# Kernel tuning notes

Measured on AMD Instinct MI355X. Metric: run time of the kernel, lower is better.

Reference implementation:

```python
import jax, jax.numpy as jnp
import numpy as np

B = 262144
L, NO, NW = 5, 5, 3          # num_layers, num_ops, num_widths
AD = L * NO * NW             # arch_dim = 75
D, H = 64, 4                 # embed_dim, num_heads
HD = D // H                  # head_dim = 16
EPS = 1e-5


def _ln(x, g, b):
    m = x.mean(-1, keepdims=True)
    v = ((x - m) ** 2).mean(-1, keepdims=True)
    return (x - m) / jnp.sqrt(v + EPS) * g + b


def setup_inputs() -> dict:
    key = jax.random.key(0)
    ks = jax.random.split(key, 16)
    s = 0.05
    return {
        "hw_idx": jax.random.randint(ks[0], (B,), 0, 4),
        "op_indices": jax.random.randint(ks[1], (B, L), 0, NO),
        "width_indices": jax.random.randint(ks[2], (B, L), 0, NW),
        "hw_embed": jax.random.normal(ks[3], (4, D)) * s,
        "W1": jax.random.normal(ks[4], (128, AD)) * s, "b1": jnp.zeros((128,)),
        "W2": jax.random.normal(ks[5], (D, 128)) * s, "b2": jnp.zeros((D,)),
        "ln1_g": jnp.ones((D,)), "ln1_b": jnp.zeros((D,)),
        "in_proj_w": jax.random.normal(ks[6], (3 * D, D)) * s,
        "in_proj_b": jnp.zeros((3 * D,)),
        "out_proj_w": jax.random.normal(ks[7], (D, D)) * s,
        "out_proj_b": jnp.zeros((D,)),
        "ln2_g": jnp.ones((D,)), "ln2_b": jnp.zeros((D,)),
        "W3": jax.random.normal(ks[8], (32, D)) * s, "b3": jnp.zeros((32,)),
        "W4": jax.random.normal(ks[9], (1, 32)) * s, "b4": jnp.zeros((1,)),
    }


def reference(hw_idx, op_indices, width_indices, hw_embed, W1, b1, W2, b2,
              ln1_g, ln1_b, in_proj_w, in_proj_b, out_proj_w, out_proj_b,
              ln2_g, ln2_b, W3, b3, W4, b4):
    # hardware embedding lookup -> [B, D]
    hw_emb = hw_embed[hw_idx]
    # vectorized one-hot arch encoding: [B, L*NO*NW]
    cell = op_indices * NW + width_indices                  # [B, L]
    onehot = jax.nn.one_hot(cell, NO * NW, dtype=jnp.float32).reshape(-1, AD)
    # arch encoder MLP + LayerNorm (dropout = identity at eval)
    h = jax.nn.relu(onehot @ W1.T + b1)
    arch_emb = _ln(h @ W2.T + b2, ln1_g, ln1_b)             # [B, D]
    # combined sequence of 2 tokens: [B, 2, D]
    combined = jnp.stack([hw_emb, arch_emb], axis=1)
    # multi-head self-attention (torch MultiheadAttention, batch_first)
    qkv = combined @ in_proj_w.T + in_proj_b                # [B, 2, 3D]
    q, k, v = jnp.split(qkv, 3, axis=-1)
    q = q.reshape(-1, 2, H, HD); k = k.reshape(-1, 2, H, HD); v = v.reshape(-1, 2, H, HD)
    scores = jnp.einsum('bqhd,bkhd->bhqk', q, k) / np.sqrt(HD)
    attn = jax.nn.softmax(scores, axis=-1)
    ctx = jnp.einsum('bhqk,bkhd->bqhd', attn, v).reshape(-1, 2, D)
    attn_out = ctx @ out_proj_w.T + out_proj_b
    # residual + LayerNorm, mean-pool over the 2 tokens
    x = _ln(attn_out + combined, ln2_g, ln2_b)
    pooled = x.mean(axis=1)                                 # [B, D]
    # prediction head
    latency = jax.nn.relu(pooled @ W3.T + b3) @ W4.T + b4   # [B, 1]
    return latency
```

## Files before the change

### kernel.cpp

```cpp
#include <hip/hip_runtime.h>


using s8v = __attribute__((ext_vector_type(8))) short;
using h8  = __attribute__((ext_vector_type(8))) _Float16;
using f4  = __attribute__((ext_vector_type(4))) float;

#define BTOT 262144

#define WF_W1   0
#define WF_W2   12288
#define WF_IP   20480
#define WF_OP   32768
#define WF_W3   36864
#define WF_HWE  38912
#define WF_ARCH 65536

__device__ __forceinline__ unsigned short f2h(float f) {
  _Float16 h = (_Float16)f;
  return __builtin_bit_cast(unsigned short, h);
}
__device__ __forceinline__ float h2f(unsigned short u) {
  return (float)__builtin_bit_cast(_Float16, u);
}

__device__ __forceinline__ void swz(const float* __restrict__ W,
                                    unsigned short* __restrict__ dst,
                                    int Kreal, int KS, int NT, int t, int stride) {
  const int total = KS * NT * 512;
  for (int i = t; i < total; i += stride) {
    const int j = i & 7, ln = (i >> 3) & 63, fr = i >> 9;
    const int nt = fr % NT, ks = fr / NT;
    const int n = nt * 16 + (ln & 15);
    const int k = ks * 32 + (ln >> 4) * 8 + j;
    dst[i] = (k < Kreal) ? f2h(W[n * Kreal + k]) : (unsigned short)0;
  }
}

__global__ void k_pre(const float* __restrict__ hwe,
                      const float* __restrict__ W1, const float* __restrict__ W2,
                      const float* __restrict__ ipw, const float* __restrict__ opw,
                      const float* __restrict__ W3,
                      unsigned short* __restrict__ ws) {
  const int t = blockIdx.x * 256 + threadIdx.x;
  const int stride = gridDim.x * 256;
  swz(W1,  ws + WF_W1, 75, 3, 8, t, stride);
  swz(W2,  ws + WF_W2, 128, 4, 4, t, stride);
  swz(ipw, ws + WF_IP, 64, 2, 12, t, stride);
  swz(opw, ws + WF_OP, 64, 2, 4, t, stride);
  swz(W3,  ws + WF_W3, 64, 2, 2, t, stride);
  for (int i = t; i < 256; i += stride) ws[WF_HWE + i] = f2h(hwe[i]);
}

__global__ __launch_bounds__(128, 3) void k_enc(
    const int* __restrict__ g_op, const int* __restrict__ g_wd,
    const float* __restrict__ g_b1, const float* __restrict__ g_b2,
    const float* __restrict__ g_ln1g, const float* __restrict__ g_ln1b,
    const unsigned short* __restrict__ wsf, unsigned short* __restrict__ g_arch) {
  __shared__ __align__(16) unsigned short sm[4608];
  const int tid = threadIdx.x;
  const int wave = tid >> 6, lane = tid & 63;
  const int quad = lane >> 4, l15 = lane & 15;
  unsigned short* pw = sm + wave * 2304;
  const int m0 = (blockIdx.x * 2 + wave) * 16;

  if (lane < 16) {
    const int smp = m0 + lane;
#pragma unroll
    for (int l = 0; l < 5; ++l) {
      const int c = 15 * l + g_op[smp * 5 + l] * 3 + g_wd[smp * 5 + l];
      pw[2176 + lane * 8 + l] = (unsigned short)c;
    }
    pw[2176 + lane * 8 + 5] = 0xFFFFu;
    pw[2176 + lane * 8 + 6] = 0xFFFFu;
    pw[2176 + lane * 8 + 7] = 0xFFFFu;
  }
  const s8v trow = *(const s8v*)(pw + 2176 + l15 * 8);

  h8 aoh[3];
#pragma unroll
  for (int ks = 0; ks < 3; ++ks) {
    s8v a;
#pragma unroll
    for (int j = 0; j < 8; ++j) {
      const int k = ks * 32 + quad * 8 + j;
      bool hit = false;
#pragma unroll
      for (int l = 0; l < 5; ++l)
        hit = hit || (k == (int)(unsigned short)trow[l]);
      a[j] = hit ? (short)0x3C00 : (short)0;
    }
    aoh[ks] = __builtin_bit_cast(h8, a);
  }

#pragma unroll
  for (int nt = 0; nt < 8; ++nt) {
    f4 acc = {0.f, 0.f, 0.f, 0.f};
#pragma unroll
    for (int ks = 0; ks < 3; ++ks) {
      const h8 bf = *(const h8*)(wsf + WF_W1 + ((ks * 8 + nt) * 64 + lane) * 8);
      acc = __builtin_amdgcn_mfma_f32_16x16x32_f16(aoh[ks], bf, acc, 0, 0, 0);
    }
    const int col = nt * 16 + l15;
    const float bias = g_b1[col];
#pragma unroll
    for (int r = 0; r < 4; ++r) {
      float v = acc[r] + bias;
      v = v > 0.f ? v : 0.f;
      pw[(quad * 4 + r) * 136 + col] = f2h(v);
    }
  }

  h8 a2[4];
#pragma unroll
  for (int ks = 0; ks < 4; ++ks)
    a2[ks] = *(const h8*)(pw + l15 * 136 + ks * 32 + quad * 8);
  f4 acc2[4];
#pragma unroll
  for (int nt = 0; nt < 4; ++nt) {
    f4 acc = {0.f, 0.f, 0.f, 0.f};
#pragma unroll
    for (int ks = 0; ks < 4; ++ks) {
      const h8 bf = *(const h8*)(wsf + WF_W2 + ((ks * 4 + nt) * 64 + lane) * 8);
      acc = __builtin_amdgcn_mfma_f32_16x16x32_f16(a2[ks], bf, acc, 0, 0, 0);
    }
    acc2[nt] = acc;
  }
  {
    float val[4][4];
#pragma unroll
    for (int nt = 0; nt < 4; ++nt) {
      const float bias = g_b2[nt * 16 + l15];
#pragma unroll
      for (int r = 0; r < 4; ++r) val[nt][r] = acc2[nt][r] + bias;
    }
#pragma unroll
    for (int r = 0; r < 4; ++r) {
      float s = val[0][r] + val[1][r] + val[2][r] + val[3][r];
      float q = val[0][r] * val[0][r] + val[1][r] * val[1][r] +
                val[2][r] * val[2][r] + val[3][r] * val[3][r];
#pragma unroll
      for (int off = 1; off <= 8; off <<= 1) {
        s += __shfl_xor(s, off);
        q += __shfl_xor(q, off);
      }
      const float mean = s * (1.f / 64.f);
      const float var  = q * (1.f / 64.f) - mean * mean;
      const float rstd = rsqrtf(var + 1e-5f);
#pragma unroll
      for (int nt = 0; nt < 4; ++nt) {
        const int col = nt * 16 + l15;
        const float gg = g_ln1g[col], bb = g_ln1b[col];
        pw[(quad * 4 + r) * 72 + col] = f2h((val[nt][r] - mean) * rstd * gg + bb);
      }
    }
  }

#pragma unroll
  for (int o = 0; o < 2; ++o) {
    const int c = o * 64 + lane;
    const int row = c >> 3, coloff = (c & 7) * 8;
    const s8v v = *(const s8v*)(pw + row * 72 + coloff);
    *(s8v*)(g_arch + (size_t)(m0 + row) * 64 + coloff) = v;
  }
}

__global__ __launch_bounds__(128, 3) void k_attn(
    const int* __restrict__ g_hw,
    const float* __restrict__ g_hwe,
    const float* __restrict__ g_ipb, const float* __restrict__ g_opb,
    const float* __restrict__ g_ln2g, const float* __restrict__ g_ln2b,
    const float* __restrict__ g_b3,  const float* __restrict__ g_W4,
    const float* __restrict__ g_b4,
    const unsigned short* __restrict__ wsf,
    float* __restrict__ g_out) {
  __shared__ __align__(16) unsigned short sm[12864];
  const int tid = threadIdx.x;
  const unsigned short* g_arch = wsf + WF_ARCH;
  const int wave = tid >> 6, lane = tid & 63;
  const int quad = lane >> 4, l15 = lane & 15;
  unsigned short* pw = sm + wave * 6432;
  const int m0 = (blockIdx.x * 2 + wave) * 16;

  if (lane < 16) pw[6400 + lane] = (unsigned short)g_hw[m0 + lane];

  const int hwrow = (int)pw[6400 + l15];
  h8 at0[2], at1[2];
#pragma unroll
  for (int ks = 0; ks < 2; ++ks) {
    at0[ks] = *(const h8*)(wsf + WF_HWE + hwrow * 64 + ks * 32 + quad * 8);
    at1[ks] = *(const h8*)(g_arch + (size_t)(m0 + l15) * 64 + ks * 32 + quad * 8);
  }
#pragma unroll
  for (int nt = 0; nt < 12; ++nt) {
    const h8 bf0 = *(const h8*)(wsf + WF_IP + ((0 * 12 + nt) * 64 + lane) * 8);
    const h8 bf1 = *(const h8*)(wsf + WF_IP + ((1 * 12 + nt) * 64 + lane) * 8);
    f4 a0 = {0.f, 0.f, 0.f, 0.f}, a1 = {0.f, 0.f, 0.f, 0.f};
    a0 = __builtin_amdgcn_mfma_f32_16x16x32_f16(at0[0], bf0, a0, 0, 0, 0);
    a0 = __builtin_amdgcn_mfma_f32_16x16x32_f16(at0[1], bf1, a0, 0, 0, 0);
    a1 = __builtin_amdgcn_mfma_f32_16x16x32_f16(at1[0], bf0, a1, 0, 0, 0);
    a1 = __builtin_amdgcn_mfma_f32_16x16x32_f16(at1[1], bf1, a1, 0, 0, 0);
    const int col = nt * 16 + l15;
    const float bias = g_ipb[col];
#pragma unroll
    for (int r = 0; r < 4; ++r) {
      pw[(quad * 4 + r) * 200 + col]      = f2h(a0[r] + bias);
      pw[(16 + quad * 4 + r) * 200 + col] = f2h(a1[r] + bias);
    }
  }

  float ctx[2][16];
  {
    float qv[2][16], kv[2][16], vv[2][16];
#pragma unroll
    for (int tt = 0; tt < 2; ++tt) {
      const unsigned short* base = pw + (tt * 16 + l15) * 200;
#pragma unroll
      for (int c = 0; c < 2; ++c) {
        const h8 qq = *(const h8*)(base + quad * 16 + c * 8);
        const h8 kk = *(const h8*)(base + 64 + quad * 16 + c * 8);
        const h8 vvv = *(const h8*)(base + 128 + quad * 16 + c * 8);
#pragma unroll
        for (int d = 0; d < 8; ++d) {
          qv[tt][c * 8 + d] = (float)qq[d];
          kv[tt][c * 8 + d] = (float)kk[d];
          vv[tt][c * 8 + d] = (float)vvv[d];
        }
      }
    }
    float s00 = 0.f, s01 = 0.f, s10 = 0.f, s11 = 0.f;
#pragma unroll
    for (int d = 0; d < 16; ++d) {
      s00 += qv[0][d] * kv[0][d];
      s01 += qv[0][d] * kv[1][d];
      s10 += qv[1][d] * kv[0][d];
      s11 += qv[1][d] * kv[1][d];
    }
    s00 *= 0.25f; s01 *= 0.25f; s10 *= 0.25f; s11 *= 0.25f;
    const float mA = fmaxf(s00, s01);
    const float e0 = __expf(s00 - mA), e1 = __expf(s01 - mA);
    const float iA = 1.f / (e0 + e1);
    const float a00 = e0 * iA, a01 = e1 * iA;
    const float mB = fmaxf(s10, s11);
    const float f0 = __expf(s10 - mB), f1 = __expf(s11 - mB);
    const float iB = 1.f / (f0 + f1);
    const float a10 = f0 * iB, a11 = f1 * iB;
#pragma unroll
    for (int d = 0; d < 16; ++d) {
      ctx[0][d] = a00 * vv[0][d] + a01 * vv[1][d];
      ctx[1][d] = a10 * vv[0][d] + a11 * vv[1][d];
    }
  }
#pragma unroll
  for (int tt = 0; tt < 2; ++tt)
#pragma unroll
    for (int d = 0; d < 16; d += 2) {
      const unsigned pk = (unsigned)f2h(ctx[tt][d]) |
                          ((unsigned)f2h(ctx[tt][d + 1]) << 16);
      *(unsigned*)(pw + (tt * 16 + l15) * 72 + quad * 16 + d) = pk;
    }

#pragma unroll
  for (int o = 0; o < 2; ++o) {
    const int c = o * 64 + lane;
    const int row = c >> 3, coloff = (c & 7) * 8;
    const s8v v = *(const s8v*)(g_arch + (size_t)(m0 + row) * 64 + coloff);
    *(s8v*)(pw + 3456 + row * 72 + coloff) = v;
  }

  h8 ca[2][2];
#pragma unroll
  for (int mt = 0; mt < 2; ++mt)
#pragma unroll
    for (int ks = 0; ks < 2; ++ks)
      ca[mt][ks] = *(const h8*)(pw + (mt * 16 + l15) * 72 + ks * 32 + quad * 8);
  f4 oacc[2][4];
#pragma unroll
  for (int nt = 0; nt < 4; ++nt) {
    const h8 bf0 = *(const h8*)(wsf + WF_OP + ((0 * 4 + nt) * 64 + lane) * 8);
    const h8 bf1 = *(const h8*)(wsf + WF_OP + ((1 * 4 + nt) * 64 + lane) * 8);
#pragma unroll
    for (int mt = 0; mt < 2; ++mt) {
      f4 acc = {0.f, 0.f, 0.f, 0.f};
      acc = __builtin_amdgcn_mfma_f32_16x16x32_f16(ca[mt][0], bf0, acc, 0, 0, 0);
      acc = __builtin_amdgcn_mfma_f32_16x16x32_f16(ca[mt][1], bf1, acc, 0, 0, 0);
      oacc[mt][nt] = acc;
    }
  }
  float pool[4][4];
#pragma unroll
  for (int mt = 0; mt < 2; ++mt) {
    float val[4][4];
#pragma unroll
    for (int nt = 0; nt < 4; ++nt) {
      const int col = nt * 16 + l15;
      const float bias = g_opb[col];
#pragma unroll
      for (int r = 0; r < 4; ++r) {
        const int row = quad * 4 + r;
        float res;
        if (mt == 0) {
          const int hr = (int)pw[6400 + row];
          res = g_hwe[hr * 64 + col];
        } else {
          res = h2f(pw[3456 + row * 72 + col]);
        }
        val[nt][r] = oacc[mt][nt][r] + bias + res;
      }
    }
#pragma unroll
    for (int r = 0; r < 4; ++r) {
      float s = val[0][r] + val[1][r] + val[2][r] + val[3][r];
      float q = val[0][r] * val[0][r] + val[1][r] * val[1][r] +
                val[2][r] * val[2][r] + val[3][r] * val[3][r];
#pragma unroll
      for (int off = 1; off <= 8; off <<= 1) {
        s += __shfl_xor(s, off);
        q += __shfl_xor(q, off);
      }
      const float mean = s * (1.f / 64.f);
      const float var  = q * (1.f / 64.f) - mean * mean;
      const float rstd = rsqrtf(var + 1e-5f);
#pragma unroll
      for (int nt = 0; nt < 4; ++nt) {
        const int col = nt * 16 + l15;
        const float gg = g_ln2g[col], bb = g_ln2b[col];
        const float xn = (val[nt][r] - mean) * rstd * gg + bb;
        if (mt == 0) pool[nt][r] = 0.5f * xn;
        else         pool[nt][r] += 0.5f * xn;
      }
    }
  }
#pragma unroll
  for (int nt = 0; nt < 4; ++nt)
#pragma unroll
    for (int r = 0; r < 4; ++r)
      pw[2304 + (quad * 4 + r) * 72 + nt * 16 + l15] = f2h(pool[nt][r]);

  h8 pa[2];
#pragma unroll
  for (int ks = 0; ks < 2; ++ks)
    pa[ks] = *(const h8*)(pw + 2304 + l15 * 72 + ks * 32 + quad * 8);
  float part[4] = {0.f, 0.f, 0.f, 0.f};
#pragma unroll
  for (int nt = 0; nt < 2; ++nt) {
    const h8 bf0 = *(const h8*)(wsf + WF_W3 + ((0 * 2 + nt) * 64 + lane) * 8);
    const h8 bf1 = *(const h8*)(wsf + WF_W3 + ((1 * 2 + nt) * 64 + lane) * 8);
    f4 acc = {0.f, 0.f, 0.f, 0.f};
    acc = __builtin_amdgcn_mfma_f32_16x16x32_f16(pa[0], bf0, acc, 0, 0, 0);
    acc = __builtin_amdgcn_mfma_f32_16x16x32_f16(pa[1], bf1, acc, 0, 0, 0);
    const int col = nt * 16 + l15;
    const float bias = g_b3[col];
    const float w4v  = g_W4[col];
#pragma unroll
    for (int r = 0; r < 4; ++r) {
      float y = acc[r] + bias;
      y = y > 0.f ? y : 0.f;
      part[r] += y * w4v;
    }
  }
#pragma unroll
  for (int off = 1; off <= 8; off <<= 1)
#pragma unroll
    for (int r = 0; r < 4; ++r)
      part[r] += __shfl_xor(part[r], off);
  const float b4v = g_b4[0];
  if (l15 == 0) {
#pragma unroll
    for (int r = 0; r < 4; ++r)
      g_out[m0 + quad * 4 + r] = part[r] + b4v;
  }
}

extern "C" void kernel_launch(void* const* d_in, const int* in_sizes, int n_in,
                              void* d_out, int out_size, void* d_ws, size_t ws_size,
                              hipStream_t stream) {
  (void)in_sizes; (void)n_in; (void)out_size; (void)ws_size;
  unsigned short* ws = (unsigned short*)d_ws;

  k_pre<<<64, 256, 0, stream>>>(
      (const float*)d_in[3], (const float*)d_in[4], (const float*)d_in[6],
      (const float*)d_in[10], (const float*)d_in[12], (const float*)d_in[16],
      ws);

  k_enc<<<8192, 128, 0, stream>>>(
      (const int*)d_in[1], (const int*)d_in[2],
      (const float*)d_in[5], (const float*)d_in[7],
      (const float*)d_in[8], (const float*)d_in[9],
      ws, ws + WF_ARCH);

  k_attn<<<8192, 128, 0, stream>>>(
      (const int*)d_in[0],
      (const float*)d_in[3],
      (const float*)d_in[11], (const float*)d_in[13],
      (const float*)d_in[14], (const float*)d_in[15],
      (const float*)d_in[17], (const float*)d_in[18],
      (const float*)d_in[19],
      ws, (float*)d_out);
}
```

Before: 177.0 us.

## Fuse arch encoder and attention kernels, keep arch embedding in LDS

Merges the encoder kernel and the attention/head kernel into one launch, so the fp16 arch embedding stays in per-wave shared memory instead of being written to and reread from global workspace. This removes a B×64 fp16 global round trip (about 32 MB of traffic each way) and one kernel launch. In exchange each wave keeps a slightly larger LDS region and the fused kernel may hold more live registers, which could affect occupancy.

New measurement: 183.5 us. +3.7%, slower.

```diff
diff --git a/kernel.cpp b/kernel.cpp
--- a/kernel.cpp
+++ b/kernel.cpp
@@ -13,7 +13,11 @@
 #define WF_OP   32768
 #define WF_W3   36864
 #define WF_HWE  38912
-#define WF_ARCH 65536
+
+#define OF_ARCH 6400
+#define OF_TARG 7552
+#define OF_HWI  7680
+#define PWS     7696
 
 __device__ __forceinline__ unsigned short f2h(float f) {
   _Float16 h = (_Float16)f;
@@ -51,144 +55,125 @@
   for (int i = t; i < 256; i += stride) ws[WF_HWE + i] = f2h(hwe[i]);
 }
 
-__global__ __launch_bounds__(128, 3) void k_enc(
+__global__ __launch_bounds__(128, 3) void k_fused(
+    const int* __restrict__ g_hw,
     const int* __restrict__ g_op, const int* __restrict__ g_wd,
+    const float* __restrict__ g_hwe,
     const float* __restrict__ g_b1, const float* __restrict__ g_b2,
     const float* __restrict__ g_ln1g, const float* __restrict__ g_ln1b,
-    const unsigned short* __restrict__ wsf, unsigned short* __restrict__ g_arch) {
-  __shared__ __align__(16) unsigned short sm[4608];
-  const int tid = threadIdx.x;
-  const int wave = tid >> 6, lane = tid & 63;
-  const int quad = lane >> 4, l15 = lane & 15;
-  unsigned short* pw = sm + wave * 2304;
-  const int m0 = (blockIdx.x * 2 + wave) * 16;
-
-  if (lane < 16) {
-    const int smp = m0 + lane;
-#pragma unroll
-    for (int l = 0; l < 5; ++l) {
-      const int c = 15 * l + g_op[smp * 5 + l] * 3 + g_wd[smp * 5 + l];
-      pw[2176 + lane * 8 + l] = (unsigned short)c;
-    }
-    pw[2176 + lane * 8 + 5] = 0xFFFFu;
-    pw[2176 + lane * 8 + 6] = 0xFFFFu;
-    pw[2176 + lane * 8 + 7] = 0xFFFFu;
-  }
-  const s8v trow = *(const s8v*)(pw + 2176 + l15 * 8);
-
-  h8 aoh[3];
-#pragma unroll
-  for (int ks = 0; ks < 3; ++ks) {
-    s8v a;
-#pragma unroll
-    for (int j = 0; j < 8; ++j) {
-      const int k = ks * 32 + quad * 8 + j;
-      bool hit = false;
-#pragma unroll
-      for (int l = 0; l < 5; ++l)
-        hit = hit || (k == (int)(unsigned short)trow[l]);
-      a[j] = hit ? (short)0x3C00 : (short)0;
-    }
-    aoh[ks] = __builtin_bit_cast(h8, a);
-  }
-
-#pragma unroll
-  for (int nt = 0; nt < 8; ++nt) {
-    f4 acc = {0.f, 0.f, 0.f, 0.f};
-#pragma unroll
-    for (int ks = 0; ks < 3; ++ks) {
-      const h8 bf = *(const h8*)(wsf + WF_W1 + ((ks * 8 + nt) * 64 + lane) * 8);
-      acc = __builtin_amdgcn_mfma_f32_16x16x32_f16(aoh[ks], bf, acc, 0, 0, 0);
-    }
-    const int col = nt * 16 + l15;
-    const float bias = g_b1[col];
-#pragma unroll
-    for (int r = 0; r < 4; ++r) {
-      float v = acc[r] + bias;
-      v = v > 0.f ? v : 0.f;
-      pw[(quad * 4 + r) * 136 + col] = f2h(v);
-    }
-  }
-
-  h8 a2[4];
-#pragma unroll
-  for (int ks = 0; ks < 4; ++ks)
-    a2[ks] = *(const h8*)(pw + l15 * 136 + ks * 32 + quad * 8);
-  f4 acc2[4];
-#pragma unroll
-  for (int nt = 0; nt < 4; ++nt) {
-    f4 acc = {0.f, 0.f, 0.f, 0.f};
-#pragma unroll
-    for (int ks = 0; ks < 4; ++ks) {
-      const h8 bf = *(const h8*)(wsf + WF_W2 + ((ks * 4 + nt) * 64 + lane) * 8);
-      acc = __builtin_amdgcn_mfma_f32_16x16x32_f16(a2[ks], bf, acc, 0, 0, 0);
-    }
-    acc2[nt] = acc;
-  }
-  {
-    float val[4][4];
-#pragma unroll
-    for (int nt = 0; nt < 4; ++nt) {
-      const float bias = g_b2[nt * 16 + l15];
-#pragma unroll
-      for (int r = 0; r < 4; ++r) val[nt][r] = acc2[nt][r] + bias;
-    }
-#pragma unroll
-    for (int r = 0; r < 4; ++r) {
-      float s = val[0][r] + val[1][r] + val[2][r] + val[3][r];
-      float q = val[0][r] * val[0][r] + val[1][r] * val[1][r] +
-                val[2][r] * val[2][r] + val[3][r] * val[3][r];
-#pragma unroll
-      for (int off = 1; off <= 8; off <<= 1) {
-        s += __shfl_xor(s, off);
-        q += __shfl_xor(q, off);
-      }
-      const float mean = s * (1.f / 64.f);
-      const float var  = q * (1.f / 64.f) - mean * mean;
-      const float rstd = rsqrtf(var + 1e-5f);
-#pragma unroll
-      for (int nt = 0; nt < 4; ++nt) {
-        const int col = nt * 16 + l15;
-        const float gg = g_ln1g[col], bb = g_ln1b[col];
-        pw[(quad * 4 + r) * 72 + col] = f2h((val[nt][r] - mean) * rstd * gg + bb);
-      }
-    }
-  }
-
-#pragma unroll
-  for (int o = 0; o < 2; ++o) {
-    const int c = o * 64 + lane;
-    const int row = c >> 3, coloff = (c & 7) * 8;
-    const s8v v = *(const s8v*)(pw + row * 72 + coloff);
-    *(s8v*)(g_arch + (size_t)(m0 + row) * 64 + coloff) = v;
-  }
-}
-
-__global__ __launch_bounds__(128, 3) void k_attn(
-    const int* __restrict__ g_hw,
-    const float* __restrict__ g_hwe,
     const float* __restrict__ g_ipb, const float* __restrict__ g_opb,
     const float* __restrict__ g_ln2g, const float* __restrict__ g_ln2b,
     const float* __restrict__ g_b3,  const float* __restrict__ g_W4,
     const float* __restrict__ g_b4,
     const unsigned short* __restrict__ wsf,
     float* __restrict__ g_out) {
-  __shared__ __align__(16) unsigned short sm[12864];
+  __shared__ __align__(16) unsigned short sm[2 * PWS];
   const int tid = threadIdx.x;
-  const unsigned short* g_arch = wsf + WF_ARCH;
   const int wave = tid >> 6, lane = tid & 63;
   const int quad = lane >> 4, l15 = lane & 15;
-  unsigned short* pw = sm + wave * 6432;
+  unsigned short* pw = sm + wave * PWS;
   const int m0 = (blockIdx.x * 2 + wave) * 16;
 
-  if (lane < 16) pw[6400 + lane] = (unsigned short)g_hw[m0 + lane];
-
-  const int hwrow = (int)pw[6400 + l15];
+  if (lane < 16) {
+    const int smp = m0 + lane;
+    pw[OF_HWI + lane] = (unsigned short)g_hw[smp];
+#pragma unroll
+    for (int l = 0; l < 5; ++l) {
+      const int c = 15 * l + g_op[smp * 5 + l] * 3 + g_wd[smp * 5 + l];
+      pw[OF_TARG + lane * 8 + l] = (unsigned short)c;
+    }
+    pw[OF_TARG + lane * 8 + 5] = 0xFFFFu;
+    pw[OF_TARG + lane * 8 + 6] = 0xFFFFu;
+    pw[OF_TARG + lane * 8 + 7] = 0xFFFFu;
+  }
+  const s8v trow = *(const s8v*)(pw + OF_TARG + l15 * 8);
+
+  h8 aoh[3];
+#pragma unroll
+  for (int ks = 0; ks < 3; ++ks) {
+    s8v a;
+#pragma unroll
+    for (int j = 0; j < 8; ++j) {
+      const int k = ks * 32 + quad * 8 + j;
+      bool hit = false;
+#pragma unroll
+      for (int l = 0; l < 5; ++l)
+        hit = hit || (k == (int)(unsigned short)trow[l]);
+      a[j] = hit ? (short)0x3C00 : (short)0;
+    }
+    aoh[ks] = __builtin_bit_cast(h8, a);
+  }
+
+#pragma unroll
+  for (int nt = 0; nt < 8; ++nt) {
+    f4 acc = {0.f, 0.f, 0.f, 0.f};
+#pragma unroll
+    for (int ks = 0; ks < 3; ++ks) {
+      const h8 bf = *(const h8*)(wsf + WF_W1 + ((ks * 8 + nt) * 64 + lane) * 8);
+      acc = __builtin_amdgcn_mfma_f32_16x16x32_f16(aoh[ks], bf, acc, 0, 0, 0);
+    }
+    const int col = nt * 16 + l15;
+    const float bias = g_b1[col];
+#pragma unroll
+    for (int r = 0; r < 4; ++r) {
+      float v = acc[r] + bias;
+      v = v > 0.f ? v : 0.f;
+      pw[(quad * 4 + r) * 136 + col] = f2h(v);
+    }
+  }
+
+  h8 a2[4];
+#pragma unroll
+  for (int ks = 0; ks < 4; ++ks)
+    a2[ks] = *(const h8*)(pw + l15 * 136 + ks * 32 + quad * 8);
+  f4 acc2[4];
+#pragma unroll
+  for (int nt = 0; nt < 4; ++nt) {
+    f4 acc = {0.f, 0.f, 0.f, 0.f};
+#pragma unroll
+    for (int ks = 0; ks < 4; ++ks) {
+      const h8 bf = *(const h8*)(wsf + WF_W2 + ((ks * 4 + nt) * 64 + lane) * 8);
+      acc = __builtin_amdgcn_mfma_f32_16x16x32_f16(a2[ks], bf, acc, 0, 0, 0);
+    }
+    acc2[nt] = acc;
+  }
+  {
+    float val[4][4];
+#pragma unroll
+    for (int nt = 0; nt < 4; ++nt) {
+      const float bias = g_b2[nt * 16 + l15];
+#pragma unroll
+      for (int r = 0; r < 4; ++r) val[nt][r] = acc2[nt][r] + bias;
+    }
+#pragma unroll
+    for (int r = 0; r < 4; ++r) {
+      float s = val[0][r] + val[1][r] + val[2][r] + val[3][r];
+      float q = val[0][r] * val[0][r] + val[1][r] * val[1][r] +
+                val[2][r] * val[2][r] + val[3][r] * val[3][r];
+#pragma unroll
+      for (int off = 1; off <= 8; off <<= 1) {
+        s += __shfl_xor(s, off);
+        q += __shfl_xor(q, off);
+      }
+      const float mean = s * (1.f / 64.f);
+      const float var  = q * (1.f / 64.f) - mean * mean;
+      const float rstd = rsqrtf(var + 1e-5f);
+#pragma unroll
+      for (int nt = 0; nt < 4; ++nt) {
+        const int col = nt * 16 + l15;
+        const float gg = g_ln1g[col], bb = g_ln1b[col];
+        pw[OF_ARCH + (quad * 4 + r) * 72 + col] =
+            f2h((val[nt][r] - mean) * rstd * gg + bb);
+      }
+    }
+  }
+
+  const int hwrow = (int)pw[OF_HWI + l15];
   h8 at0[2], at1[2];
 #pragma unroll
   for (int ks = 0; ks < 2; ++ks) {
     at0[ks] = *(const h8*)(wsf + WF_HWE + hwrow * 64 + ks * 32 + quad * 8);
-    at1[ks] = *(const h8*)(g_arch + (size_t)(m0 + l15) * 64 + ks * 32 + quad * 8);
+    at1[ks] = *(const h8*)(pw + OF_ARCH + l15 * 72 + ks * 32 + quad * 8);
   }
 #pragma unroll
   for (int nt = 0; nt < 12; ++nt) {
@@ -259,14 +244,6 @@
       *(unsigned*)(pw + (tt * 16 + l15) * 72 + quad * 16 + d) = pk;
     }
 
-#pragma unroll
-  for (int o = 0; o < 2; ++o) {
-    const int c = o * 64 + lane;
-    const int row = c >> 3, coloff = (c & 7) * 8;
-    const s8v v = *(const s8v*)(g_arch + (size_t)(m0 + row) * 64 + coloff);
-    *(s8v*)(pw + 3456 + row * 72 + coloff) = v;
-  }
-
   h8 ca[2][2];
 #pragma unroll
   for (int mt = 0; mt < 2; ++mt)
@@ -299,10 +276,10 @@
         const int row = quad * 4 + r;
         float res;
         if (mt == 0) {
-          const int hr = (int)pw[6400 + row];
+          const int hr = (int)pw[OF_HWI + row];
           res = g_hwe[hr * 64 + col];
         } else {
-          res = h2f(pw[3456 + row * 72 + col]);
+          res = h2f(pw[OF_ARCH + row * 72 + col]);
         }
         val[nt][r] = oacc[mt][nt][r] + bias + res;
       }
@@ -382,15 +359,12 @@
       (const float*)d_in[10], (const float*)d_in[12], (const float*)d_in[16],
       ws);
 
-  k_enc<<<8192, 128, 0, stream>>>(
+  k_fused<<<8192, 128, 0, stream>>>(
+      (const int*)d_in[0],
       (const int*)d_in[1], (const int*)d_in[2],
+      (const float*)d_in[3],
       (const float*)d_in[5], (const float*)d_in[7],
       (const float*)d_in[8], (const float*)d_in[9],
-      ws, ws + WF_ARCH);
-
-  k_attn<<<8192, 128, 0, stream>>>(
-      (const int*)d_in[0],
-      (const float*)d_in[3],
       (const float*)d_in[11], (const float*)d_in[13],
       (const float*)d_in[14], (const float*)d_in[15],
       (const float*)d_in[17], (const float*)d_in[18],
```
